# Optimization experiments

Measured on AMD Instinct MI355X. Metric: run time of the kernel, lower is better.

## Reference

```python
import jax, jax.numpy as jnp
import numpy as np

N = 4096
D_IN = 1024
D_Q = 1024
D_V = 1024

def setup_inputs() -> dict:
    key = jax.random.key(0)
    ks = jax.random.split(key, 8)
    # x scaled down a bit so exp() of raw (unstable, no max-subtract) scores stays finite,
    # matching the original module's numerics regime.
    x = jax.random.normal(ks[0], (N, D_IN), dtype=jnp.float32) * 0.02
    mask = jax.random.uniform(ks[1], (N, N), dtype=jnp.float32)
    s = 1.0 / np.sqrt(D_IN)
    Wq = jax.random.normal(ks[2], (D_IN, D_Q), dtype=jnp.float32) * s
    bq = jax.random.normal(ks[3], (D_Q,), dtype=jnp.float32) * 0.02
    Wk = jax.random.normal(ks[4], (D_IN, D_Q), dtype=jnp.float32) * s
    bk = jax.random.normal(ks[5], (D_Q,), dtype=jnp.float32) * 0.02
    Wv = jax.random.normal(ks[6], (D_IN, D_V), dtype=jnp.float32) * s
    bv = jax.random.normal(ks[7], (D_V,), dtype=jnp.float32) * 0.02
    return {"x": x, "mask": mask, "Wq": Wq, "bq": bq, "Wk": Wk, "bk": bk, "Wv": Wv, "bv": bv}

def reference(x, mask, Wq, bq, Wk, bk, Wv, bv):
    # Q, K, V projections (nn.Linear: x @ W + b, here W stored as [in, out])
    Q = x @ Wq + bq          # [N, Dq]
    K = x @ Wk + bk          # [N, Dq]
    V = x @ Wv + bv          # [N, Dv]
    scale = 1.0              # default scale in original forward
    scores = scale * (Q @ K.T)   # [N, N]
    scores = mask * scores       # elementwise multiplicative mask
    # Faithful to original (quirky) normalization:
    # exp(S) / sum(exp(S), axis=1)[None, :]  -> row-sums broadcast across ROWS
    e = jnp.exp(scores)                       # [N, N]
    denom = jnp.sum(e, axis=1)[None, :]       # [1, N]
    softmax = e / denom                       # [N, N]
    return softmax @ V                        # [N, Dv]
```

## Files before the change

kernel.cpp:

```cpp
#include <hip/hip_runtime.h>
#include <hip/hip_bf16.h>


#define N_TOK 4096
#define D_DIM 1024
#define VS_SCALE 131072.0f

typedef __bf16 bf16x8 __attribute__((ext_vector_type(8)));
typedef __bf16 bf16x4 __attribute__((ext_vector_type(4)));
typedef float  f32x4  __attribute__((ext_vector_type(4)));

typedef const __attribute__((address_space(1))) char g_char;
typedef __attribute__((address_space(3))) char lds_char;

__device__ inline unsigned char f32_to_fp8(float f) {
    return (unsigned char)(__builtin_amdgcn_cvt_pk_fp8_f32(f, f, 0, false) & 0xff);
}

__global__ void cvt_and_bias(const float* __restrict__ x, __bf16* __restrict__ xb,
                             const float* __restrict__ bq, const float* __restrict__ bk,
                             const float* __restrict__ bv, float* __restrict__ bcat) {
    int b = blockIdx.x;
    if (b < 4096) {
        int i = (b * 256 + threadIdx.x) * 4;
        float4 v = *(const float4*)(x + i);
        bf16x4 o;
        o.x = (__bf16)v.x; o.y = (__bf16)v.y;
        o.z = (__bf16)v.z; o.w = (__bf16)v.w;
        *(bf16x4*)(xb + i) = o;
    } else {
        int i = (b - 4096) * 256 + threadIdx.x;
        if (i < 1024) bcat[i] = bq[i];
        else if (i < 2048) bcat[i] = bk[i - 1024];
        else if (i < 3072) bcat[i] = bv[i - 2048];
    }
}

__global__ void transpose_w3(const float* __restrict__ Wq, const float* __restrict__ Wk,
                             const float* __restrict__ Wv, __bf16* __restrict__ outT) {
    const float* in = (blockIdx.z == 0) ? Wq : (blockIdx.z == 1) ? Wk : Wv;
    __bf16* oT = outT + (size_t)blockIdx.z * 1024 * 1024;
    __shared__ float t[64][65];
    const int c0 = blockIdx.x * 64, r0 = blockIdx.y * 64;
    const int tid = threadIdx.x;
#pragma unroll
    for (int k = 0; k < 16; k++) {
        int lin = tid + k * 256;
        int r = lin >> 6, c = lin & 63;
        t[r][c] = in[(size_t)(r0 + r) * 1024 + c0 + c];
    }
    __syncthreads();
#pragma unroll
    for (int k = 0; k < 16; k++) {
        int lin = tid + k * 256;
        int c = lin >> 6, r = lin & 63;
        oT[(size_t)(c0 + c) * 1024 + r0 + r] = (__bf16)t[r][c];
    }
}

__global__ void scale_transpose(const __bf16* __restrict__ V, int ldv,
                                const float* __restrict__ denom,
                                unsigned char* __restrict__ VT8) {
    __shared__ float t[64][65];
    __shared__ float rd[64];
    const int d0 = blockIdx.x * 64, j0 = blockIdx.y * 64;
    const int tid = threadIdx.x;
    if (tid < 64) rd[tid] = VS_SCALE / denom[j0 + tid];
    __syncthreads();
#pragma unroll
    for (int k = 0; k < 16; k++) {
        int lin = tid + k * 256;
        int j = lin >> 6, d = lin & 63;
        t[j][d] = (float)V[(size_t)(j0 + j) * ldv + d0 + d] * rd[j];
    }
    __syncthreads();
#pragma unroll
    for (int k = 0; k < 16; k++) {
        int lin = tid + k * 256;
        int d = lin >> 6, j = lin & 63;
        VT8[(size_t)(d0 + d) * N_TOK + j0 + j] = f32_to_fp8(t[j][d]);
    }
}

template <int EPI>
__global__ __launch_bounds__(512, 2)
void gemm_nt_256(const __bf16* __restrict__ A, const __bf16* __restrict__ B,
                 int lda, int ldb, int ldc, int K,
                 const float* __restrict__ bias,
                 const float* __restrict__ mask,
                 __bf16* __restrict__ Cb, unsigned char* __restrict__ C8,
                 float* __restrict__ denom) {
    __shared__ __bf16 ldsb[2 * 32768];

    const int tid  = threadIdx.x;
    const int wave = tid >> 6;
    const int lane = tid & 63;
    const int quad = lane >> 4;
    const int l16  = lane & 15;
    const int l7   = l16 & 7;
    const int m0 = blockIdx.y * 256;
    const int n0 = blockIdx.x * 256;
    const int wr = (wave >> 2) * 128;
    const int wc = (wave & 3) * 64;

    const size_t lda_b = (size_t)lda * 2;
    const size_t ldb_b = (size_t)ldb * 2;
    const int tr = tid >> 3;
    const int ts = ((tid & 7) ^ (tr & 7)) * 16;
    const char* gA = (const char*)A + (size_t)(m0 + tr) * lda_b + ts;
    const char* gB = (const char*)B + (size_t)(n0 + tr) * ldb_b + ts;
    const size_t rstepA = (size_t)64 * lda_b;
    const size_t rstepB = (size_t)64 * ldb_b;

    lds_char* lw = (lds_char*)(void*)ldsb + wave * 1024;

    const int s0 = ((0 + quad) ^ l7) * 16;
    const int s1 = ((4 + quad) ^ l7) * 16;
    const int aRow = (wr + l16) * 128;
    const int bRow = (wc + l16) * 128 + 32768;

    f32x4 acc[8][4];
#pragma unroll
    for (int i = 0; i < 8; i++)
#pragma unroll
        for (int j = 0; j < 4; j++) acc[i][j] = (f32x4){0.f, 0.f, 0.f, 0.f};

    const int NT = K >> 6;

#define STAGE4(tt, bb, gg) do {                                                       \
    const char* ga_ = gA + (size_t)(tt) * 128 + (size_t)(2 * (gg)) * rstepA;          \
    const char* gb_ = gB + (size_t)(tt) * 128 + (size_t)(2 * (gg)) * rstepB;          \
    lds_char* la_ = lw + (bb) * 65536 + (2 * (gg)) * 8192;                            \
    lds_char* lb_ = lw + (bb) * 65536 + 32768 + (2 * (gg)) * 8192;                    \
    __builtin_amdgcn_global_load_lds((g_char*)(ga_),          la_,        16, 0, 0);  \
    __builtin_amdgcn_global_load_lds((g_char*)(ga_ + rstepA), la_ + 8192, 16, 0, 0);  \
    __builtin_amdgcn_global_load_lds((g_char*)(gb_),          lb_,        16, 0, 0);  \
    __builtin_amdgcn_global_load_lds((g_char*)(gb_ + rstepB), lb_ + 8192, 16, 0, 0);  \
} while (0)

    STAGE4(0, 0, 0);
    STAGE4(0, 0, 1);
    asm volatile("s_waitcnt vmcnt(0)" ::: "memory");
    __builtin_amdgcn_s_barrier();

    for (int t = 0; t < NT; ++t) {
        const int cb = t & 1;
        const char* buf = (const char*)ldsb + cb * 65536;
        const bool pf = (t + 1 < NT);
        bf16x8 bfr[4][2];

#pragma unroll
        for (int p = 0; p < 4; p++) {
            if (p == 0) {
#pragma unroll
                for (int j = 0; j < 4; j++) {
                    bfr[j][0] = *(const bf16x8*)(buf + bRow + j * 2048 + s0);
                    bfr[j][1] = *(const bf16x8*)(buf + bRow + j * 2048 + s1);
                }
            }
            bf16x8 aF[2][2];
#pragma unroll
            for (int ii = 0; ii < 2; ii++) {
                aF[ii][0] = *(const bf16x8*)(buf + aRow + (2 * p + ii) * 2048 + s0);
                aF[ii][1] = *(const bf16x8*)(buf + aRow + (2 * p + ii) * 2048 + s1);
            }
            if (p < 2 && pf) STAGE4(t + 1, cb ^ 1, p);

            __builtin_amdgcn_s_barrier();
            asm volatile("s_waitcnt lgkmcnt(0)" ::: "memory");
            __builtin_amdgcn_sched_barrier(0);
            __builtin_amdgcn_s_setprio(1);
#pragma unroll
            for (int ii = 0; ii < 2; ii++)
#pragma unroll
                for (int j = 0; j < 4; j++) {
                    acc[2 * p + ii][j] = __builtin_amdgcn_mfma_f32_16x16x32_bf16(
                        aF[ii][0], bfr[j][0], acc[2 * p + ii][j], 0, 0, 0);
                    acc[2 * p + ii][j] = __builtin_amdgcn_mfma_f32_16x16x32_bf16(
                        aF[ii][1], bfr[j][1], acc[2 * p + ii][j], 0, 0, 0);
                }
            __builtin_amdgcn_s_setprio(0);
            __builtin_amdgcn_sched_barrier(0);
            if (p == 3) asm volatile("s_waitcnt vmcnt(0)" ::: "memory");
            __builtin_amdgcn_s_barrier();
        }
    }
#undef STAGE4

#pragma unroll
    for (int i = 0; i < 8; i++) {
        const int rbase = m0 + wr + i * 16 + quad * 4;
        f32x4 rs = (f32x4){0.f, 0.f, 0.f, 0.f};
#pragma unroll
        for (int j = 0; j < 4; j++) {
            const int col = n0 + wc + j * 16 + l16;
            f32x4 v = acc[i][j];
            if (EPI == 0) {
                const float bb = bias[col];
#pragma unroll
                for (int r = 0; r < 4; r++)
                    Cb[(size_t)(rbase + r) * ldc + col] = (__bf16)(v[r] + bb);
            } else {
#pragma unroll
                for (int r = 0; r < 4; r++) {
                    size_t idx = (size_t)(rbase + r) * ldc + col;
                    float e = __expf(mask[idx] * v[r]);
                    C8[idx] = f32_to_fp8(e);
                    rs[r] += e;
                }
            }
        }
        if (EPI == 1) {
#pragma unroll
            for (int m = 1; m < 16; m <<= 1) {
#pragma unroll
                for (int r = 0; r < 4; r++) rs[r] += __shfl_xor(rs[r], m, 64);
            }
            if (l16 == 0) {
#pragma unroll
                for (int r = 0; r < 4; r++) atomicAdd(&denom[rbase + r], rs[r]);
            }
        }
    }
}

__global__ __launch_bounds__(256, 2)
void gemm_out_fp8(const unsigned char* __restrict__ A,
                  const unsigned char* __restrict__ B,
                  float* __restrict__ C) {
    __shared__ unsigned char lA[128 * 128];
    __shared__ unsigned char lB[64 * 128];

    const int tid  = threadIdx.x;
    const int wave = tid >> 6;
    const int lane = tid & 63;
    const int quad = lane >> 4;
    const int l16  = lane & 15;
    const int m0 = blockIdx.y * 128;
    const int n0 = blockIdx.x * 64;
    const int wr = (wave >> 1) * 64;
    const int wc = (wave & 1) * 32;

    const int tr = tid >> 3;
    const int ts = ((tid & 7) ^ (tr & 7)) * 16;
    const char* gA = (const char*)A + (size_t)(m0 + tr) * N_TOK + ts;
    const char* gB = (const char*)B + (size_t)(n0 + tr) * N_TOK + ts;
    const size_t pstep = (size_t)32 * N_TOK;

    lds_char* lAp = (lds_char*)(void*)lA + wave * 1024;
    lds_char* lBp = (lds_char*)(void*)lB + wave * 1024;

    const int l7 = l16 & 7;
    const int qhi = quad >> 1, qlo = (quad & 1) * 8;
    int rdA[4], rdB[4];
#pragma unroll
    for (int k = 0; k < 4; k++) {
        rdA[k] = ((k * 2 + qhi) ^ l7) * 16 + qlo;
        rdB[k] = rdA[k];
    }

    f32x4 acc[4][2];
#pragma unroll
    for (int i = 0; i < 4; i++)
#pragma unroll
        for (int j = 0; j < 2; j++) acc[i][j] = (f32x4){0.f, 0.f, 0.f, 0.f};

    for (int kt = 0; kt < N_TOK; kt += 128) {
#pragma unroll
        for (int c = 0; c < 4; c++)
            __builtin_amdgcn_global_load_lds((g_char*)(gA + c * pstep),
                                             lAp + c * 4096, 16, 0, 0);
#pragma unroll
        for (int c = 0; c < 2; c++)
            __builtin_amdgcn_global_load_lds((g_char*)(gB + c * pstep),
                                             lBp + c * 4096, 16, 0, 0);
        gA += 128;
        gB += 128;
        __syncthreads();

#pragma unroll
        for (int k = 0; k < 4; k++) {
            long a[4], b[2];
#pragma unroll
            for (int i = 0; i < 4; i++)
                a[i] = *(const long*)&lA[(wr + i * 16 + l16) * 128 + rdA[k]];
#pragma unroll
            for (int j = 0; j < 2; j++)
                b[j] = *(const long*)&lB[(wc + j * 16 + l16) * 128 + rdB[k]];
#pragma unroll
            for (int i = 0; i < 4; i++)
#pragma unroll
                for (int j = 0; j < 2; j++)
                    acc[i][j] = __builtin_amdgcn_mfma_f32_16x16x32_fp8_fp8(
                        a[i], b[j], acc[i][j], 0, 0, 0);
        }
        __syncthreads();
    }

#pragma unroll
    for (int i = 0; i < 4; i++) {
#pragma unroll
        for (int j = 0; j < 2; j++) {
            const int col   = n0 + wc + j * 16 + l16;
            const int rbase = m0 + wr + i * 16 + quad * 4;
            f32x4 v = acc[i][j];
#pragma unroll
            for (int r = 0; r < 4; r++)
                C[(size_t)(rbase + r) * D_DIM + col] = v[r] * (1.0f / VS_SCALE);
        }
    }
}

extern "C" void kernel_launch(void* const* d_in, const int* in_sizes, int n_in,
                              void* d_out, int out_size, void* d_ws, size_t ws_size,
                              hipStream_t stream) {
    const float* x    = (const float*)d_in[0];
    const float* mask = (const float*)d_in[1];
    const float* Wq   = (const float*)d_in[2];
    const float* bq   = (const float*)d_in[3];
    const float* Wk   = (const float*)d_in[4];
    const float* bk   = (const float*)d_in[5];
    const float* Wv   = (const float*)d_in[6];
    const float* bv   = (const float*)d_in[7];
    float* out = (float*)d_out;
    char* ws = (char*)d_ws;

    const size_t MB = 1024 * 1024;
    unsigned char* E8   = (unsigned char*)(ws + 0 * MB);
    __bf16* QKVb  = (__bf16*)(ws + 16 * MB);
    __bf16* xb    = (__bf16*)(ws + 40 * MB);
    unsigned char* VsT8 = (unsigned char*)xb;
    __bf16* WcatT = (__bf16*)(ws + 48 * MB);
    float*  bcat  = (float*)(ws + 54 * MB);
    float*  denom = (float*)(ws + 54 * MB + 64 * 1024);

    hipMemsetAsync(denom, 0, N_TOK * sizeof(float), stream);

    cvt_and_bias<<<4096 + 12, 256, 0, stream>>>(x, xb, bq, bk, bv, bcat);
    transpose_w3<<<dim3(16, 16, 3), 256, 0, stream>>>(Wq, Wk, Wv, WcatT);

    gemm_nt_256<0><<<dim3(12, 16), 512, 0, stream>>>(
        xb, WcatT, D_DIM, D_DIM, 3 * D_DIM, D_DIM,
        bcat, nullptr, QKVb, nullptr, nullptr);

    const __bf16* Qb = QKVb;
    const __bf16* Kb = QKVb + D_DIM;
    gemm_nt_256<1><<<dim3(16, 16), 512, 0, stream>>>(
        Qb, Kb, 3 * D_DIM, 3 * D_DIM, N_TOK, D_DIM,
        nullptr, mask, nullptr, E8, denom);

    scale_transpose<<<dim3(16, 64), 256, 0, stream>>>(QKVb + 2048, 3 * D_DIM, denom, VsT8);

    gemm_out_fp8<<<dim3(16, 32), 256, 0, stream>>>(E8, VsT8, out);
}
```

Baseline: 252.2 us.

## Use 4-stage K=32 LDS ring pipeline with grouped block swizzle in GEMM

Replaces the double-buffered K=64 mainloop with a four-slot ring of K=32 stages, kept three loads ahead and gated by partial vmcnt waits, with one barrier per stage instead of eight per tile. It also remaps workgroup IDs so groups of eight consecutive blocks share tiles for better L2 reuse, and changes the LDS swizzle to suit 64-byte rows. The aim is to hide global load latency and cut barrier overhead. In exchange, the pipeline is deeper, stages are smaller, and correctness now depends on the hand-counted vmcnt values and on the grid size being divisible by eight.

```diff
diff --git a/kernel.cpp b/kernel.cpp
--- a/kernel.cpp
+++ b/kernel.cpp
@@ -90,34 +90,39 @@
                  const float* __restrict__ mask,
                  __bf16* __restrict__ Cb, unsigned char* __restrict__ C8,
                  float* __restrict__ denom) {
-    __shared__ __bf16 ldsb[2 * 32768];
+    __shared__ __bf16 ldsb[4 * 16384];
 
     const int tid  = threadIdx.x;
     const int wave = tid >> 6;
     const int lane = tid & 63;
     const int quad = lane >> 4;
     const int l16  = lane & 15;
-    const int l7   = l16 & 7;
-    const int m0 = blockIdx.y * 256;
-    const int n0 = blockIdx.x * 256;
+
+    const int nbx = gridDim.x;
+    const int nwg = gridDim.x * gridDim.y;
+    const int bid = blockIdx.y * nbx + blockIdx.x;
+    const int cpx = nwg >> 3;
+    const int swz = (bid & 7) * cpx + (bid >> 3);
+    const int m0 = (swz / nbx) * 256;
+    const int n0 = (swz % nbx) * 256;
+
     const int wr = (wave >> 2) * 128;
     const int wc = (wave & 3) * 64;
 
     const size_t lda_b = (size_t)lda * 2;
     const size_t ldb_b = (size_t)ldb * 2;
-    const int tr = tid >> 3;
-    const int ts = ((tid & 7) ^ (tr & 7)) * 16;
-    const char* gA = (const char*)A + (size_t)(m0 + tr) * lda_b + ts;
-    const char* gB = (const char*)B + (size_t)(n0 + tr) * ldb_b + ts;
-    const size_t rstepA = (size_t)64 * lda_b;
-    const size_t rstepB = (size_t)64 * ldb_b;
-
-    lds_char* lw = (lds_char*)(void*)ldsb + wave * 1024;
-
-    const int s0 = ((0 + quad) ^ l7) * 16;
-    const int s1 = ((4 + quad) ^ l7) * 16;
-    const int aRow = (wr + l16) * 128;
-    const int bRow = (wc + l16) * 128 + 32768;
+    const int trow = tid >> 2;
+    const int tcs  = ((tid & 3) ^ ((tid >> 3) & 3)) * 16;
+    const char* gA = (const char*)A + (size_t)(m0 + trow) * lda_b + tcs;
+    const char* gB = (const char*)B + (size_t)(n0 + trow) * ldb_b + tcs;
+    const size_t rstepA = 128 * lda_b;
+    const size_t rstepB = 128 * ldb_b;
+
+    lds_char* lw = (lds_char*)(void*)ldsb + tid * 16;
+
+    const int cswz = (quad ^ ((l16 >> 1) & 3)) * 16;
+    const int aOff = (wr + l16) * 64 + cswz;
+    const int bOff = (wc + l16) * 64 + cswz + 16384;
 
     f32x4 acc[8][4];
 #pragma unroll
@@ -125,67 +130,48 @@
 #pragma unroll
         for (int j = 0; j < 4; j++) acc[i][j] = (f32x4){0.f, 0.f, 0.f, 0.f};
 
-    const int NT = K >> 6;
-
-#define STAGE4(tt, bb, gg) do {                                                       \
-    const char* ga_ = gA + (size_t)(tt) * 128 + (size_t)(2 * (gg)) * rstepA;          \
-    const char* gb_ = gB + (size_t)(tt) * 128 + (size_t)(2 * (gg)) * rstepB;          \
-    lds_char* la_ = lw + (bb) * 65536 + (2 * (gg)) * 8192;                            \
-    lds_char* lb_ = lw + (bb) * 65536 + 32768 + (2 * (gg)) * 8192;                    \
-    __builtin_amdgcn_global_load_lds((g_char*)(ga_),          la_,        16, 0, 0);  \
-    __builtin_amdgcn_global_load_lds((g_char*)(ga_ + rstepA), la_ + 8192, 16, 0, 0);  \
-    __builtin_amdgcn_global_load_lds((g_char*)(gb_),          lb_,        16, 0, 0);  \
-    __builtin_amdgcn_global_load_lds((g_char*)(gb_ + rstepB), lb_ + 8192, 16, 0, 0);  \
+    const int H = K >> 5;
+
+#define STAGEH(hh) do {                                                              \
+    const char* ga_ = gA + (size_t)(hh) * 64;                                        \
+    const char* gb_ = gB + (size_t)(hh) * 64;                                        \
+    lds_char* ls_ = lw + ((hh) & 3) * 32768;                                         \
+    __builtin_amdgcn_global_load_lds((g_char*)(ga_),          ls_,          16, 0, 0); \
+    __builtin_amdgcn_global_load_lds((g_char*)(ga_ + rstepA), ls_ + 8192,   16, 0, 0); \
+    __builtin_amdgcn_global_load_lds((g_char*)(gb_),          ls_ + 16384,  16, 0, 0); \
+    __builtin_amdgcn_global_load_lds((g_char*)(gb_ + rstepB), ls_ + 24576,  16, 0, 0); \
 } while (0)
 
-    STAGE4(0, 0, 0);
-    STAGE4(0, 0, 1);
-    asm volatile("s_waitcnt vmcnt(0)" ::: "memory");
-    __builtin_amdgcn_s_barrier();
-
-    for (int t = 0; t < NT; ++t) {
-        const int cb = t & 1;
-        const char* buf = (const char*)ldsb + cb * 65536;
-        const bool pf = (t + 1 < NT);
-        bf16x8 bfr[4][2];
-
-#pragma unroll
-        for (int p = 0; p < 4; p++) {
-            if (p == 0) {
-#pragma unroll
-                for (int j = 0; j < 4; j++) {
-                    bfr[j][0] = *(const bf16x8*)(buf + bRow + j * 2048 + s0);
-                    bfr[j][1] = *(const bf16x8*)(buf + bRow + j * 2048 + s1);
-                }
-            }
-            bf16x8 aF[2][2];
-#pragma unroll
-            for (int ii = 0; ii < 2; ii++) {
-                aF[ii][0] = *(const bf16x8*)(buf + aRow + (2 * p + ii) * 2048 + s0);
-                aF[ii][1] = *(const bf16x8*)(buf + aRow + (2 * p + ii) * 2048 + s1);
-            }
-            if (p < 2 && pf) STAGE4(t + 1, cb ^ 1, p);
-
-            __builtin_amdgcn_s_barrier();
-            asm volatile("s_waitcnt lgkmcnt(0)" ::: "memory");
-            __builtin_amdgcn_sched_barrier(0);
-            __builtin_amdgcn_s_setprio(1);
-#pragma unroll
-            for (int ii = 0; ii < 2; ii++)
-#pragma unroll
-                for (int j = 0; j < 4; j++) {
-                    acc[2 * p + ii][j] = __builtin_amdgcn_mfma_f32_16x16x32_bf16(
-                        aF[ii][0], bfr[j][0], acc[2 * p + ii][j], 0, 0, 0);
-                    acc[2 * p + ii][j] = __builtin_amdgcn_mfma_f32_16x16x32_bf16(
-                        aF[ii][1], bfr[j][1], acc[2 * p + ii][j], 0, 0, 0);
-                }
-            __builtin_amdgcn_s_setprio(0);
-            __builtin_amdgcn_sched_barrier(0);
-            if (p == 3) asm volatile("s_waitcnt vmcnt(0)" ::: "memory");
-            __builtin_amdgcn_s_barrier();
-        }
-    }
-#undef STAGE4
+    STAGEH(0);
+    STAGEH(1);
+    STAGEH(2);
+
+    for (int h = 0; h < H; ++h) {
+        if (h + 2 < H)      asm volatile("s_waitcnt vmcnt(8)" ::: "memory");
+        else if (h + 1 < H) asm volatile("s_waitcnt vmcnt(4)" ::: "memory");
+        else                asm volatile("s_waitcnt vmcnt(0)" ::: "memory");
+        __builtin_amdgcn_s_barrier();
+        __builtin_amdgcn_sched_barrier(0);
+        if (h + 3 < H) STAGEH(h + 3);
+
+        const char* sb = (const char*)ldsb + (h & 3) * 32768;
+        bf16x8 af[8], bfr[4];
+#pragma unroll
+        for (int i = 0; i < 8; i++) af[i] = *(const bf16x8*)(sb + aOff + i * 1024);
+#pragma unroll
+        for (int j = 0; j < 4; j++) bfr[j] = *(const bf16x8*)(sb + bOff + j * 1024);
+
+        __builtin_amdgcn_s_setprio(1);
+#pragma unroll
+        for (int i = 0; i < 8; i++)
+#pragma unroll
+            for (int j = 0; j < 4; j++)
+                acc[i][j] = __builtin_amdgcn_mfma_f32_16x16x32_bf16(
+                    af[i], bfr[j], acc[i][j], 0, 0, 0);
+        __builtin_amdgcn_s_setprio(0);
+        __builtin_amdgcn_sched_barrier(0);
+    }
+#undef STAGEH
 
 #pragma unroll
     for (int i = 0; i < 8; i++) {
```

Measured after the change: 249.6 us. Within noise of the previous version (-1.0%).
